# Kernel tuning notes

Hardware: AMD Instinct MI355X
Metric: run time of the kernel (lower is better)

Reference implementation:

```python
import jax, jax.numpy as jnp
import numpy as np

N_NODES = 100000
N_EDGES = 1600000
D_IN = 128
D_HID = 128
D_OUT = 10
N_GRAPHS = 512


def setup_inputs() -> dict:
    key = jax.random.key(0)
    ks = jax.random.split(key, 12)
    x = jax.random.normal(ks[0], (N_NODES, D_IN), dtype=jnp.float32)
    edge_index = jax.random.randint(ks[1], (2, N_EDGES), 0, N_NODES, dtype=jnp.int64)
    batch = jnp.sort(jax.random.randint(ks[2], (N_NODES,), 0, N_GRAPHS, dtype=jnp.int64))
    s = 1.0 / np.sqrt(D_HID)
    W0 = jax.random.normal(ks[3], (D_HID, D_IN), dtype=jnp.float32) * s
    b0 = jax.random.normal(ks[4], (D_HID,), dtype=jnp.float32) * s
    W1 = jax.random.normal(ks[5], (D_HID, D_HID), dtype=jnp.float32) * s
    b1 = jax.random.normal(ks[6], (D_HID,), dtype=jnp.float32) * s
    W2 = jax.random.normal(ks[7], (D_HID, D_HID), dtype=jnp.float32) * s
    b2 = jax.random.normal(ks[8], (D_HID,), dtype=jnp.float32) * s
    Wg = jax.random.normal(ks[9], (D_OUT, D_HID), dtype=jnp.float32) * s
    bg = jax.random.normal(ks[10], (D_OUT,), dtype=jnp.float32) * s
    return {"x": x, "edge_index": edge_index, "batch": batch,
            "W0": W0, "b0": b0, "W1": W1, "b1": b1, "W2": W2, "b2": b2,
            "Wg": Wg, "bg": bg}


def _gin_conv(x, src, dst, W, b):
    # GINConv with eps=0: Linear(x + sum_{j in N(i)} x_j)
    agg = jax.ops.segment_sum(x[src], dst, num_segments=N_NODES)  # [N, d]
    return (x + agg) @ W.T + b


def reference(x, edge_index, batch, W0, b0, W1, b1, W2, b2, Wg, bg):
    src, dst = edge_index[0], edge_index[1]
    h = jax.nn.relu(_gin_conv(x, src, dst, W0, b0))
    h = jax.nn.relu(_gin_conv(h, src, dst, W1, b1))
    h = _gin_conv(h, src, dst, W2, b2)
    # global_mean_pool over graph ids
    sums = jax.ops.segment_sum(h, batch, num_segments=N_GRAPHS)            # [G, d]
    counts = jax.ops.segment_sum(jnp.ones((N_NODES,), h.dtype), batch, num_segments=N_GRAPHS)
    pooled = sums / jnp.maximum(counts, 1.0)[:, None]                       # [G, d]
    return pooled @ Wg.T + bg                                               # [G, out]
```

## Files before the change

kernel.cpp:

```cpp
#include <hip/hip_runtime.h>

#define N_NODES 100000
#define N_EDGES 1600000
#define N_GRAPHS 512
#define NBUCK 391
#define EPB 2048
#define NB_SCAT ((N_EDGES + EPB - 1) / EPB)
#define CAPB 4864
#define CONV_BLKS 6250

typedef _Float16 half8 __attribute__((ext_vector_type(8)));
typedef float floatx4 __attribute__((ext_vector_type(4)));

union U16 { uint4 u; half8 h; };

__global__ __launch_bounds__(256) void convert_pack(const float4* __restrict__ X4,
                                                    uint4* __restrict__ Xh,
                                                    const float* __restrict__ W0,
                                                    const float* __restrict__ W1,
                                                    const float* __restrict__ W2,
                                                    uint4* __restrict__ Bp,
                                                    int* __restrict__ gcur) {
    int bid = blockIdx.x, tid = threadIdx.x;
    if (bid < CONV_BLKS) {
        int t = bid * 256 + tid;
        float4 a = X4[t * 2], b = X4[t * 2 + 1];
        U16 o;
        o.h[0] = (_Float16)a.x; o.h[1] = (_Float16)a.y;
        o.h[2] = (_Float16)a.z; o.h[3] = (_Float16)a.w;
        o.h[4] = (_Float16)b.x; o.h[5] = (_Float16)b.y;
        o.h[6] = (_Float16)b.z; o.h[7] = (_Float16)b.w;
        Xh[t] = o.u;
    } else {
        int zi = (bid - CONV_BLKS) * 256 + tid;
        if (zi < NBUCK) gcur[zi] = 0;
        int slice = (bid - CONV_BLKS) * 4 + (tid >> 6);
        if (slice >= 96) return;
        int l = tid & 63;
        int layer = slice >> 5;
        int r = slice & 31;
        int c = r >> 3, f = r & 7;
        const float* W = (layer == 0) ? W0 : (layer == 1) ? W1 : W2;
        int col = f * 16 + (l & 15);
        int k0 = c * 32 + (l >> 4) * 8;
        U16 o;
        #pragma unroll
        for (int j = 0; j < 8; ++j) o.h[j] = (_Float16)W[col * 128 + k0 + j];
        Bp[layer * 2048 + (c * 8 + f) * 64 + l] = o.u;
    }
}

__global__ __launch_bounds__(256) void bucket_scatter(const int* __restrict__ src,
                                                      const int* __restrict__ dst,
                                                      int* __restrict__ gcur,
                                                      unsigned* __restrict__ pairs) {
    __shared__ int cnt[NBUCK];
    __shared__ int base[NBUCK];
    int tid = threadIdx.x;
    for (int i = tid; i < NBUCK; i += 256) cnt[i] = 0;
    __syncthreads();
    int e0 = blockIdx.x * EPB, e1 = min(e0 + EPB, N_EDGES);
    for (int e = e0 + tid; e < e1; e += 256) atomicAdd(&cnt[dst[e] >> 8], 1);
    __syncthreads();
    for (int i = tid; i < NBUCK; i += 256) {
        int v = cnt[i];
        base[i] = i * CAPB + (v ? atomicAdd(&gcur[i], v) : 0);
        cnt[i] = 0;
    }
    __syncthreads();
    for (int e = e0 + tid; e < e1; e += 256) {
        int d = dst[e], b = d >> 8;
        int r = atomicAdd(&cnt[b], 1);
        pairs[base[b] + r] = (unsigned)src[e] | ((unsigned)(d & 255) << 17);
    }
}

__global__ __launch_bounds__(256) void bucket_fine(const unsigned* __restrict__ pairs,
                                                   const int* __restrict__ gcur,
                                                   int* __restrict__ off,
                                                   int* __restrict__ srclist) {
    __shared__ int snap[NBUCK];
    __shared__ int ncnt[256];
    __shared__ int ws[4];
    int tid = threadIdx.x, b = blockIdx.x;
    int lane = tid & 63, w = tid >> 6;

    for (int i = tid; i < NBUCK; i += 256) snap[i] = gcur[i];
    ncnt[tid] = 0;
    __syncthreads();
    if (tid < 64) {
        int carry = 0;
        for (int base = 0; base < NBUCK; base += 64) {
            int i = base + tid;
            int v = (i < NBUCK) ? snap[i] : 0;
            int incl = v;
            #pragma unroll
            for (int s = 1; s < 64; s <<= 1) {
                int y = __shfl_up(incl, s, 64);
                if (tid >= s) incl += y;
            }
            if (i < NBUCK) snap[i] = carry + incl - v;
            carry += __shfl(incl, 63, 64);
        }
    }
    __syncthreads();
    int eLo = snap[b];
    int eNext = (b == NBUCK - 1) ? N_EDGES : snap[b + 1];
    int m = eNext - eLo;
    int sb = b * CAPB;
    if (b == 0 && tid == 0) off[N_NODES] = N_EDGES;
    __syncthreads();

    for (int t = tid; t < m; t += 256) {
        unsigned p = pairs[sb + t];
        atomicAdd(&ncnt[(p >> 17) & 255], 1);
    }
    __syncthreads();
    int v = ncnt[tid];
    int incl = v;
    #pragma unroll
    for (int s = 1; s < 64; s <<= 1) { int y = __shfl_up(incl, s, 64); if (lane >= s) incl += y; }
    if (lane == 63) ws[w] = incl;
    __syncthreads();
    if (tid < 4) {
        int t = ws[tid];
        #pragma unroll
        for (int s = 1; s < 4; s <<= 1) { int y = __shfl_up(t, s, 64); if (tid >= s) t += y; }
        ws[tid] = t;
    }
    __syncthreads();
    int excl = (w ? ws[w - 1] : 0) + incl - v;
    int n = (b << 8) + tid;
    if (n < N_NODES) off[n] = eLo + excl;
    __syncthreads();
    ncnt[tid] = excl;
    __syncthreads();
    for (int t = tid; t < m; t += 256) {
        unsigned p = pairs[sb + t];
        int r = atomicAdd(&ncnt[(p >> 17) & 255], 1);
        srclist[eLo + r] = (int)(p & 0x1FFFFu);
    }
}

__global__ __launch_bounds__(256) void agg_f16(const uint4* __restrict__ Xh,
                                               uint4* __restrict__ Ah,
                                               const int* __restrict__ off,
                                               const int* __restrict__ srclist) {
    int t = blockIdx.x * 256 + threadIdx.x;
    int n = t >> 4, c = t & 15;
    if (n >= N_NODES) return;
    int j0 = off[n], j1 = off[n + 1];
    U16 acc; acc.u = Xh[(size_t)n * 16 + c];
    half8 a = acc.h;
    int j = j0;
    for (; j + 3 < j1; j += 4) {
        int s0 = srclist[j], s1 = srclist[j + 1], s2 = srclist[j + 2], s3 = srclist[j + 3];
        U16 v0, v1, v2, v3;
        v0.u = Xh[(size_t)s0 * 16 + c];
        v1.u = Xh[(size_t)s1 * 16 + c];
        v2.u = Xh[(size_t)s2 * 16 + c];
        v3.u = Xh[(size_t)s3 * 16 + c];
        a += v0.h; a += v1.h; a += v2.h; a += v3.h;
    }
    for (; j < j1; ++j) {
        U16 v; v.u = Xh[(size_t)srclist[j] * 16 + c];
        a += v.h;
    }
    U16 o; o.h = a;
    Ah[(size_t)n * 16 + c] = o.u;
}

__global__ __launch_bounds__(256) void gemm_mfma(const _Float16* __restrict__ Ah,
                                                 const uint4* __restrict__ Bp,
                                                 const float* __restrict__ bias,
                                                 _Float16* __restrict__ H, int doRelu) {
    int tid = threadIdx.x;
    int wid = tid >> 6, lane = tid & 63;
    int nbase = blockIdx.x * 64 + wid * 16;
    int lrow = lane & 15;
    int lk = (lane >> 4) * 8;
    int row0 = min(nbase + lrow, N_NODES - 1);

    floatx4 acc[8];
    #pragma unroll
    for (int f = 0; f < 8; ++f) acc[f] = (floatx4)0.f;

    #pragma unroll
    for (int c = 0; c < 4; ++c) {
        U16 a0;
        a0.u = *(const uint4*)(Ah + (size_t)row0 * 128 + c * 32 + lk);
        #pragma unroll
        for (int f = 0; f < 8; ++f) {
            U16 b; b.u = Bp[(c * 8 + f) * 64 + lane];
            acc[f] = __builtin_amdgcn_mfma_f32_16x16x32_f16(b.h, a0.h, acc[f], 0, 0, 0);
        }
    }

    int ncol = lane & 15;
    int rq = (lane >> 4) * 4;
    int node = nbase + ncol;
    if (node >= N_NODES) return;
    #pragma unroll
    for (int f = 0; f < 8; ++f) {
        float4 bv = *(const float4*)(bias + f * 16 + rq);
        float o0 = acc[f][0] + bv.x;
        float o1 = acc[f][1] + bv.y;
        float o2 = acc[f][2] + bv.z;
        float o3 = acc[f][3] + bv.w;
        if (doRelu) {
            o0 = fmaxf(o0, 0.f); o1 = fmaxf(o1, 0.f);
            o2 = fmaxf(o2, 0.f); o3 = fmaxf(o3, 0.f);
        }
        ushort4 st;
        st.x = (unsigned short)__builtin_bit_cast(unsigned short, (_Float16)o0);
        st.y = (unsigned short)__builtin_bit_cast(unsigned short, (_Float16)o1);
        st.z = (unsigned short)__builtin_bit_cast(unsigned short, (_Float16)o2);
        st.w = (unsigned short)__builtin_bit_cast(unsigned short, (_Float16)o3);
        *(ushort4*)(H + (size_t)node * 128 + f * 16 + rq) = st;
    }
}

__device__ __forceinline__ int lower_bound_i(const int* a, int n, int val) {
    int lo = 0, hi = n;
    while (lo < hi) {
        int mid = (lo + hi) >> 1;
        if (a[mid] < val) lo = mid + 1; else hi = mid;
    }
    return lo;
}

__global__ __launch_bounds__(256) void pool_kernel(const uint4* __restrict__ Hh,
                                                   const int* __restrict__ batch,
                                                   const float* __restrict__ Wg,
                                                   const float* __restrict__ bg,
                                                   float* __restrict__ out) {
    __shared__ float p[16 * 128];
    __shared__ float pooled[128];
    int g = blockIdx.x, tid = threadIdx.x;
    int c = tid & 15, r = tid >> 4;
    int lo = lower_bound_i(batch, N_NODES, g);
    int hi = lower_bound_i(batch, N_NODES, g + 1);
    float acc[8] = {0, 0, 0, 0, 0, 0, 0, 0};
    for (int i = lo + r; i < hi; i += 16) {
        U16 v; v.u = Hh[(size_t)i * 16 + c];
        #pragma unroll
        for (int k = 0; k < 8; ++k) acc[k] += (float)v.h[k];
    }
    #pragma unroll
    for (int k = 0; k < 8; ++k) p[r * 128 + c * 8 + k] = acc[k];
    __syncthreads();
    if (tid < 128) {
        float s = 0.f;
        #pragma unroll
        for (int q = 0; q < 16; ++q) s += p[q * 128 + tid];
        pooled[tid] = s / fmaxf((float)(hi - lo), 1.0f);
    }
    __syncthreads();
    if (tid < 10) {
        float s = bg[tid];
        #pragma unroll 4
        for (int k = 0; k < 128; ++k) s += pooled[k] * Wg[tid * 128 + k];
        out[g * 10 + tid] = s;
    }
}

extern "C" void kernel_launch(void* const* d_in, const int* in_sizes, int n_in,
                              void* d_out, int out_size, void* d_ws, size_t ws_size,
                              hipStream_t stream) {
    const float* x   = (const float*)d_in[0];
    const int*   ei  = (const int*)d_in[1];
    const int*   bat = (const int*)d_in[2];
    const float* W0  = (const float*)d_in[3];
    const float* b0  = (const float*)d_in[4];
    const float* W1  = (const float*)d_in[5];
    const float* b1  = (const float*)d_in[6];
    const float* W2  = (const float*)d_in[7];
    const float* b2  = (const float*)d_in[8];
    const float* Wg  = (const float*)d_in[9];
    const float* bg  = (const float*)d_in[10];
    float* out = (float*)d_out;

    const int* src = ei;
    const int* dst = ei + N_EDGES;

    char* w = (char*)d_ws;
    _Float16* Ah    = (_Float16*)(w);
    unsigned* pairs = (unsigned*)(w);
    _Float16* P0    = (_Float16*)(w + 25600000);
    _Float16* P1    = (_Float16*)(w + 51200000);
    _Float16* P2    = (_Float16*)(w + 76800000);
    int*    srclist = (int*)(w + 102400000);
    int*    off     = (int*)(w + 108800000);
    uint4*  Bp      = (uint4*)(w + 109300000);
    int*    gcur    = (int*)(w + 109450000);

    convert_pack<<<CONV_BLKS + 24, 256, 0, stream>>>((const float4*)x, (uint4*)P0,
                                                     W0, W1, W2, Bp, gcur);
    bucket_scatter<<<NB_SCAT, 256, 0, stream>>>(src, dst, gcur, pairs);
    bucket_fine<<<NBUCK, 256, 0, stream>>>(pairs, gcur, off, srclist);

    int aggGrid  = (N_NODES * 16 + 255) / 256;
    int gemmGrid = (N_NODES + 63) / 64;

    agg_f16<<<aggGrid, 256, 0, stream>>>((const uint4*)P0, (uint4*)Ah, off, srclist);
    gemm_mfma<<<gemmGrid, 256, 0, stream>>>(Ah, Bp, b0, P1, 1);
    agg_f16<<<aggGrid, 256, 0, stream>>>((const uint4*)P1, (uint4*)Ah, off, srclist);
    gemm_mfma<<<gemmGrid, 256, 0, stream>>>(Ah, Bp + 2048, b1, P2, 1);
    agg_f16<<<aggGrid, 256, 0, stream>>>((const uint4*)P2, (uint4*)Ah, off, srclist);
    gemm_mfma<<<gemmGrid, 256, 0, stream>>>(Ah, Bp + 4096, b2, P0, 0);

    pool_kernel<<<N_GRAPHS, 256, 0, stream>>>((const uint4*)P0, bat, Wg, bg, out);
}
```

Before: 327.3 us.

## Fuse neighbor aggregation and MFMA linear layer into one kernel per GIN layer

Merges the fp16 gather-sum aggregation and the MFMA GEMM into a single kernel per layer. Each 256-thread block aggregates 16 nodes into padded LDS, then its four waves each compute two 16-column output tiles from that LDS tile. This removes the write and re-read of the intermediate aggregated activation buffer and three kernel launches. In exchange, every block reloads the full packed weight matrix from global or L2 for only 16 rows, and the grid assumes N_NODES divides evenly by 16.

```diff
diff --git a/kernel.cpp b/kernel.cpp
--- a/kernel.cpp
+++ b/kernel.cpp
@@ -142,13 +142,20 @@
     }
 }
 
-__global__ __launch_bounds__(256) void agg_f16(const uint4* __restrict__ Xh,
-                                               uint4* __restrict__ Ah,
-                                               const int* __restrict__ off,
-                                               const int* __restrict__ srclist) {
-    int t = blockIdx.x * 256 + threadIdx.x;
-    int n = t >> 4, c = t & 15;
-    if (n >= N_NODES) return;
+__global__ __launch_bounds__(256) void gin_fused(const uint4* __restrict__ Xh,
+                                                 const uint4* __restrict__ Bp,
+                                                 const float* __restrict__ bias,
+                                                 _Float16* __restrict__ H,
+                                                 const int* __restrict__ off,
+                                                 const int* __restrict__ srclist,
+                                                 int doRelu) {
+    __shared__ ushort lds[16 * 136];
+    int tid = threadIdx.x;
+    int n0 = blockIdx.x * 16;
+    int r = tid >> 4;
+    int c = tid & 15;
+    int n = n0 + r;
+
     int j0 = off[n], j1 = off[n + 1];
     U16 acc; acc.u = Xh[(size_t)n * 16 + c];
     half8 a = acc.h;
@@ -167,46 +174,38 @@
         a += v.h;
     }
     U16 o; o.h = a;
-    Ah[(size_t)n * 16 + c] = o.u;
-}
-
-__global__ __launch_bounds__(256) void gemm_mfma(const _Float16* __restrict__ Ah,
-                                                 const uint4* __restrict__ Bp,
-                                                 const float* __restrict__ bias,
-                                                 _Float16* __restrict__ H, int doRelu) {
-    int tid = threadIdx.x;
+    *(uint4*)&lds[r * 136 + c * 8] = o.u;
+    __syncthreads();
+
     int wid = tid >> 6, lane = tid & 63;
-    int nbase = blockIdx.x * 64 + wid * 16;
     int lrow = lane & 15;
-    int lk = (lane >> 4) * 8;
-    int row0 = min(nbase + lrow, N_NODES - 1);
-
-    floatx4 acc[8];
+    int lk8 = (lane >> 4) * 8;
+
+    floatx4 acc2[2];
+    acc2[0] = (floatx4)0.f;
+    acc2[1] = (floatx4)0.f;
     #pragma unroll
-    for (int f = 0; f < 8; ++f) acc[f] = (floatx4)0.f;
-
-    #pragma unroll
-    for (int c = 0; c < 4; ++c) {
-        U16 a0;
-        a0.u = *(const uint4*)(Ah + (size_t)row0 * 128 + c * 32 + lk);
-        #pragma unroll
-        for (int f = 0; f < 8; ++f) {
-            U16 b; b.u = Bp[(c * 8 + f) * 64 + lane];
-            acc[f] = __builtin_amdgcn_mfma_f32_16x16x32_f16(b.h, a0.h, acc[f], 0, 0, 0);
+    for (int c4 = 0; c4 < 4; ++c4) {
+        U16 af; af.u = *(const uint4*)&lds[lrow * 136 + c4 * 32 + lk8];
+        #pragma unroll
+        for (int q = 0; q < 2; ++q) {
+            int f = wid * 2 + q;
+            U16 b; b.u = Bp[(c4 * 8 + f) * 64 + lane];
+            acc2[q] = __builtin_amdgcn_mfma_f32_16x16x32_f16(b.h, af.h, acc2[q], 0, 0, 0);
         }
     }
 
     int ncol = lane & 15;
     int rq = (lane >> 4) * 4;
-    int node = nbase + ncol;
-    if (node >= N_NODES) return;
+    int node = n0 + ncol;
     #pragma unroll
-    for (int f = 0; f < 8; ++f) {
+    for (int q = 0; q < 2; ++q) {
+        int f = wid * 2 + q;
         float4 bv = *(const float4*)(bias + f * 16 + rq);
-        float o0 = acc[f][0] + bv.x;
-        float o1 = acc[f][1] + bv.y;
-        float o2 = acc[f][2] + bv.z;
-        float o3 = acc[f][3] + bv.w;
+        float o0 = acc2[q][0] + bv.x;
+        float o1 = acc2[q][1] + bv.y;
+        float o2 = acc2[q][2] + bv.z;
+        float o3 = acc2[q][3] + bv.w;
         if (doRelu) {
             o0 = fmaxf(o0, 0.f); o1 = fmaxf(o1, 0.f);
             o2 = fmaxf(o2, 0.f); o3 = fmaxf(o3, 0.f);
@@ -284,7 +283,6 @@
     const int* dst = ei + N_EDGES;
 
     char* w = (char*)d_ws;
-    _Float16* Ah    = (_Float16*)(w);
     unsigned* pairs = (unsigned*)(w);
     _Float16* P0    = (_Float16*)(w + 25600000);
     _Float16* P1    = (_Float16*)(w + 51200000);
@@ -299,15 +297,11 @@
     bucket_scatter<<<NB_SCAT, 256, 0, stream>>>(src, dst, gcur, pairs);
     bucket_fine<<<NBUCK, 256, 0, stream>>>(pairs, gcur, off, srclist);
 
-    int aggGrid  = (N_NODES * 16 + 255) / 256;
-    int gemmGrid = (N_NODES + 63) / 64;
-
-    agg_f16<<<aggGrid, 256, 0, stream>>>((const uint4*)P0, (uint4*)Ah, off, srclist);
-    gemm_mfma<<<gemmGrid, 256, 0, stream>>>(Ah, Bp, b0, P1, 1);
-    agg_f16<<<aggGrid, 256, 0, stream>>>((const uint4*)P1, (uint4*)Ah, off, srclist);
-    gemm_mfma<<<gemmGrid, 256, 0, stream>>>(Ah, Bp + 2048, b1, P2, 1);
-    agg_f16<<<aggGrid, 256, 0, stream>>>((const uint4*)P2, (uint4*)Ah, off, srclist);
-    gemm_mfma<<<gemmGrid, 256, 0, stream>>>(Ah, Bp + 4096, b2, P0, 0);
+    int grid = N_NODES / 16;
+
+    gin_fused<<<grid, 256, 0, stream>>>((const uint4*)P0, Bp, b0, P1, off, srclist, 1);
+    gin_fused<<<grid, 256, 0, stream>>>((const uint4*)P1, Bp + 2048, b1, P2, off, srclist, 1);
+    gin_fused<<<grid, 256, 0, stream>>>((const uint4*)P2, Bp + 4096, b2, P0, off, srclist, 0);
 
     pool_kernel<<<N_GRAPHS, 256, 0, stream>>>((const uint4*)P0, bat, Wg, bg, out);
 }
```

Measured after the change: 282.6 us (median of 2 runs). 1.16x faster.
